# Kernel optimization log

Measured on AMD Instinct MI355X. Metric: run time of the kernel, lower is better.

Reference implementation:

```python
import jax, jax.numpy as jnp
import numpy as np

N_C, N_T, N_D = 50000, 30000, 20000
N = N_C + N_T + N_D
R = 4          # num relations
E_R = 400000   # edges per relation (contiguous blocks in edge_index)
L = 2          # num layers
H = 256        # hidden dim
EPS = 1e-5


def _layernorm(x, g, b):
    mu = jnp.mean(x, axis=-1, keepdims=True)
    var = jnp.mean(jnp.square(x - mu), axis=-1, keepdims=True)
    return (x - mu) * jax.lax.rsqrt(var + EPS) * g + b


def setup_inputs() -> dict:
    key = jax.random.key(0)
    ks = jax.random.split(key, 16)
    s = 0.02
    return {
        "x_compound": jax.random.normal(ks[0], (N_C, 256), jnp.float32),
        "x_target": jax.random.normal(ks[1], (N_T, 512), jnp.float32),
        "x_disease": jax.random.normal(ks[2], (N_D, 128), jnp.float32),
        "edge_index": jax.random.randint(ks[3], (2, R * E_R), 0, N, jnp.int32),
        "Wp_compound": jax.random.normal(ks[4], (256, H), jnp.float32) * s,
        "bp_compound": jnp.zeros((H,), jnp.float32),
        "Wp_target": jax.random.normal(ks[5], (512, H), jnp.float32) * s,
        "bp_target": jnp.zeros((H,), jnp.float32),
        "Wp_disease": jax.random.normal(ks[6], (128, H), jnp.float32) * s,
        "bp_disease": jnp.zeros((H,), jnp.float32),
        "rgcn_w": jax.random.normal(ks[7], (L, R, H, H), jnp.float32) * s,
        "rgcn_root": jax.random.normal(ks[8], (L, H, H), jnp.float32) * s,
        "rgcn_b": jnp.zeros((L, H), jnp.float32),
        "ln_g": jnp.ones((L, H), jnp.float32),
        "ln_b": jnp.zeros((L, H), jnp.float32),
        "Wo": jax.random.normal(ks[9], (H, H), jnp.float32) * s,
        "bo": jnp.zeros((H,), jnp.float32),
    }


def reference(x_compound, x_target, x_disease, edge_index,
              Wp_compound, bp_compound, Wp_target, bp_target,
              Wp_disease, bp_disease, rgcn_w, rgcn_root, rgcn_b,
              ln_g, ln_b, Wo, bo):
    # input projections per entity type, then concat (dict -> combined tensor)
    h = jnp.concatenate([
        x_compound @ Wp_compound + bp_compound,
        x_target @ Wp_target + bp_target,
        x_disease @ Wp_disease + bp_disease,
    ], axis=0)  # [N, H]

    for l in range(L):
        # RGCNConv (num_bases=None, aggr='add'): root transform + per-relation scatter-add
        out = h @ rgcn_root[l] + rgcn_b[l]
        for r in range(R):
            src = edge_index[0, r * E_R:(r + 1) * E_R]
            dst = edge_index[1, r * E_R:(r + 1) * E_R]
            msg = (h @ rgcn_w[l, r])[src]                 # [E_R, H] gather
            out = out + jax.ops.segment_sum(msg, dst, num_segments=N)
        if l > 0:  # residual only for layer_idx > 0
            out = out + h
        out = _layernorm(out, ln_g[l], ln_b[l])
        # dropout is identity in eval mode
        h = out

    y = h @ Wo + bo
    return (y[:N_C], y[N_C:N_C + N_T], y[N_C + N_T:])
```

## Files before the change

kernel.cpp:

```cpp
#include <hip/hip_runtime.h>
#include <hip/hip_bf16.h>

namespace {
constexpr int kNC = 50000;
constexpr int kNT = 30000;
constexpr int kND = 20000;
constexpr int kN  = 100000;
constexpr int kR  = 4;
constexpr int kER = 400000;
constexpr int kE  = kR * kER;
constexpr int kH  = 256;
constexpr int kB  = kR * kN;

constexpr int padM(int m) { return (m + 127) / 128 * 128; }
}

typedef __attribute__((ext_vector_type(8))) short short8;
typedef __attribute__((ext_vector_type(4))) float f32x4;
typedef __attribute__((ext_vector_type(4))) unsigned short us4;

__device__ __forceinline__ unsigned short f2bf(float x) {
    unsigned u = __builtin_bit_cast(unsigned, x);
    u += 0x7FFF + ((u >> 16) & 1);
    return (unsigned short)(u >> 16);
}
__device__ __forceinline__ float bf2f(unsigned short u) {
    unsigned v = ((unsigned)u) << 16;
    return __builtin_bit_cast(float, v);
}
__device__ __forceinline__ float bf2f_s(short u) {
    unsigned v = ((unsigned)(unsigned short)u) << 16;
    return __builtin_bit_cast(float, v);
}

__device__ __forceinline__ void gld16(const void* src, void* lds) {
    __builtin_amdgcn_global_load_lds(
        (const __attribute__((address_space(1))) void*)src,
        (__attribute__((address_space(3))) void*)lds, 16, 0, 0);
}

__device__ __forceinline__ us4 ld_u4(const unsigned short* p) {
    return *reinterpret_cast<const us4*>(p);
}
__device__ __forceinline__ void nt_store_f(float* p, float v) {
    __builtin_nontemporal_store(v, p);
}

__global__ __launch_bounds__(256)
void gemm_mfma(const unsigned short* __restrict__ A, int lda,
               const unsigned short* __restrict__ Bt, int ldb,
               const float* __restrict__ bias,
               float* __restrict__ Cf, unsigned short* __restrict__ Cb,
               int M, int K, int accumulate)
{
    __shared__ __attribute__((aligned(16))) unsigned short As[128 * 32];
    __shared__ __attribute__((aligned(16))) unsigned short Bs[128 * 32];
    const int tid  = threadIdx.x;
    const int lane = tid & 63;
    const int wid  = tid >> 6;
    const int wm   = wid >> 1;
    const int wn   = wid & 1;
    const int row0 = blockIdx.y * 128;
    const int col0 = blockIdx.x * 128;

    const int cr = lane >> 2;
    const int cs = lane & 3;

    const f32x4 z4 = {0.f, 0.f, 0.f, 0.f};
    f32x4 acc[4][4];
    #pragma unroll
    for (int m = 0; m < 4; ++m)
        #pragma unroll
        for (int n = 0; n < 4; ++n) acc[m][n] = z4;

    const int fr = lane & 15;
    const int kb = lane >> 4;

    for (int k0 = 0; k0 < K; k0 += 32) {
        #pragma unroll
        for (int j = 0; j < 2; ++j) {
            const int chunk = wid * 2 + j;
            const int r  = chunk * 16 + cr;
            const int sg = cs ^ ((r >> 1) & 3);
            gld16(A  + (size_t)(row0 + r) * lda + k0 + sg * 8, As + chunk * 512);
            gld16(Bt + (size_t)(col0 + r) * ldb + k0 + sg * 8, Bs + chunk * 512);
        }
        __syncthreads();
        short8 a[4], b[4];
        #pragma unroll
        for (int m = 0; m < 4; ++m) {
            const int am = wm * 64 + m * 16 + fr;
            const int s  = kb ^ ((am >> 1) & 3);
            a[m] = *(const short8*)(As + am * 32 + s * 8);
        }
        #pragma unroll
        for (int n = 0; n < 4; ++n) {
            const int bn = wn * 64 + n * 16 + fr;
            const int s  = kb ^ ((bn >> 1) & 3);
            b[n] = *(const short8*)(Bs + bn * 32 + s * 8);
        }
        #pragma unroll
        for (int m = 0; m < 4; ++m)
            #pragma unroll
            for (int n = 0; n < 4; ++n)
                acc[m][n] = __builtin_amdgcn_mfma_f32_16x16x32_bf16(
                    a[m], b[n], acc[m][n], 0, 0, 0);
        __syncthreads();
    }

    const int fq = lane >> 4;
    #pragma unroll
    for (int m = 0; m < 4; ++m) {
        #pragma unroll
        for (int n = 0; n < 4; ++n) {
            const int col  = col0 + wn * 64 + n * 16 + fr;
            const int rowb = row0 + wm * 64 + m * 16 + fq * 4;
            const float bv = bias ? bias[col] : 0.0f;
            #pragma unroll
            for (int i = 0; i < 4; ++i) {
                const int row = rowb + i;
                if (row >= M) continue;
                const float v = acc[m][n][i] + bv;
                const size_t idx = (size_t)row * kH + col;
                if (Cb) Cb[idx] = f2bf(v);
                else if (accumulate) Cf[idx] += v;
                else nt_store_f(&Cf[idx], v);
            }
        }
    }
}

__global__ __launch_bounds__(256, 4)
void rgcn_fused(const unsigned short* __restrict__ h_cur,
                const int* __restrict__ off, const int* __restrict__ esort,
                const unsigned short* __restrict__ W2,
                const float* __restrict__ bias, const float* __restrict__ g,
                const float* __restrict__ b,
                unsigned short* __restrict__ h_nxt, int useResid)
{
    __shared__ __attribute__((aligned(16))) unsigned short A_seg[32 * 256];
    __shared__ float red[2][4][32];
    __shared__ float gcol[256], bcol[256], biascol[256];

    const int tid  = threadIdx.x;
    const int lane = tid & 63;
    const int wid  = tid >> 6;
    const int row0 = blockIdx.x * 32;
    const int fr   = lane & 15;
    const int kb   = lane >> 4;
    const int eg   = lane >> 4;
    const int sl   = lane & 15;

    gcol[tid] = g[tid]; bcol[tid] = b[tid]; biascol[tid] = bias[tid];

    const f32x4 z4 = {0.f, 0.f, 0.f, 0.f};
    f32x4 acc[2][4];
    #pragma unroll
    for (int m = 0; m < 2; ++m)
        #pragma unroll
        for (int n = 0; n < 4; ++n) acc[m][n] = z4;

    char* const aBase = reinterpret_cast<char*>(A_seg);

    for (int p = 0; p < 5; ++p) {
        __syncthreads();
        if (p < 4) {
            int offv = 0;
            if (lane < 9) {
                int d = row0 + wid * 8 + lane;
                offv = off[(size_t)p * kN + d];
            }
            #pragma unroll
            for (int batch = 0; batch < 2; ++batch) {
                const int wrow = wid * 8 + batch * 4 + eg;
                const int t0 = __shfl(offv, batch * 4 + eg);
                const int t1 = __shfl(offv, batch * 4 + eg + 1);
                float a[16];
                #pragma unroll
                for (int i = 0; i < 16; ++i) a[i] = 0.f;
                int t = t0;
                for (; t + 2 <= t1; t += 2) {
                    const int s0 = esort[t];
                    const int s1 = esort[t + 1];
                    const short8 v0a = *reinterpret_cast<const short8*>(
                        h_cur + (size_t)s0 * kH + sl * 16);
                    const short8 v0b = *reinterpret_cast<const short8*>(
                        h_cur + (size_t)s0 * kH + sl * 16 + 8);
                    const short8 v1a = *reinterpret_cast<const short8*>(
                        h_cur + (size_t)s1 * kH + sl * 16);
                    const short8 v1b = *reinterpret_cast<const short8*>(
                        h_cur + (size_t)s1 * kH + sl * 16 + 8);
                    #pragma unroll
                    for (int i = 0; i < 8; ++i) {
                        a[i]     += bf2f_s(v0a[i]) + bf2f_s(v1a[i]);
                        a[8 + i] += bf2f_s(v0b[i]) + bf2f_s(v1b[i]);
                    }
                }
                if (t < t1) {
                    const int s0 = esort[t];
                    const short8 v0a = *reinterpret_cast<const short8*>(
                        h_cur + (size_t)s0 * kH + sl * 16);
                    const short8 v0b = *reinterpret_cast<const short8*>(
                        h_cur + (size_t)s0 * kH + sl * 16 + 8);
                    #pragma unroll
                    for (int i = 0; i < 8; ++i) {
                        a[i]     += bf2f_s(v0a[i]);
                        a[8 + i] += bf2f_s(v0b[i]);
                    }
                }
                short8 w0, w1;
                #pragma unroll
                for (int i = 0; i < 8; ++i) {
                    w0[i] = (short)f2bf(a[i]);
                    w1[i] = (short)f2bf(a[8 + i]);
                }
                const int byte0 = (wrow * 512 + sl * 32) ^ ((wrow & 7) << 4);
                *reinterpret_cast<short8*>(aBase + byte0) = w0;
                *reinterpret_cast<short8*>(aBase + (byte0 ^ 16)) = w1;
            }
        } else {
            #pragma unroll
            for (int i = 0; i < 4; ++i) {
                const int base = i * 4096 + wid * 1024;
                const int o = base + lane * 16;
                const int row = o >> 9;
                const int offr = (o & 511) ^ ((row & 7) << 4);
                gld16(h_cur + (size_t)(row0 + row) * kH + (offr >> 1), aBase + base);
            }
        }
        __syncthreads();

        const unsigned short* Wp = W2 + (size_t)p * 8 * 8192;
        #pragma unroll
        for (int ks = 0; ks < 8; ++ks) {
            const unsigned short* Wks = Wp + ks * 8192;
            const int kByte = ks * 64 + kb * 16;
            short8 a[2], bf[4];
            #pragma unroll
            for (int m = 0; m < 2; ++m) {
                const int am = m * 16 + fr;
                const int byte = (am * 512 + kByte) ^ ((am & 7) << 4);
                a[m] = *reinterpret_cast<const short8*>(aBase + byte);
            }
            #pragma unroll
            for (int n = 0; n < 4; ++n) {
                const int cn = wid * 64 + n * 16 + fr;
                bf[n] = *reinterpret_cast<const short8*>(Wks + cn * 32 + kb * 8);
            }
            #pragma unroll
            for (int m = 0; m < 2; ++m)
                #pragma unroll
                for (int n = 0; n < 4; ++n)
                    acc[m][n] = __builtin_amdgcn_mfma_f32_16x16x32_bf16(
                        a[m], bf[n], acc[m][n], 0, 0, 0);
        }
    }

    const int fq = lane >> 4;
    #pragma unroll
    for (int m = 0; m < 2; ++m) {
        #pragma unroll
        for (int i = 0; i < 4; ++i) {
            const int rowloc = m * 16 + fq * 4 + i;
            const int row = row0 + rowloc;
            float s = 0.f, q = 0.f;
            #pragma unroll
            for (int n = 0; n < 4; ++n) {
                const int col = wid * 64 + n * 16 + fr;
                float v = acc[m][n][i] + biascol[col];
                if (useResid) v += bf2f(h_cur[(size_t)row * kH + col]);
                acc[m][n][i] = v;
                s += v;
                q += v * v;
            }
            #pragma unroll
            for (int w = 1; w <= 8; w <<= 1) {
                s += __shfl_xor(s, w);
                q += __shfl_xor(q, w);
            }
            if (fr == 0) { red[0][wid][rowloc] = s; red[1][wid][rowloc] = q; }
        }
    }
    __syncthreads();
    #pragma unroll
    for (int m = 0; m < 2; ++m) {
        #pragma unroll
        for (int i = 0; i < 4; ++i) {
            const int rowloc = m * 16 + fq * 4 + i;
            const int row = row0 + rowloc;
            const float s  = red[0][0][rowloc] + red[0][1][rowloc]
                           + red[0][2][rowloc] + red[0][3][rowloc];
            const float qq = red[1][0][rowloc] + red[1][1][rowloc]
                           + red[1][2][rowloc] + red[1][3][rowloc];
            const float mu = s * (1.0f / kH);
            const float var = qq * (1.0f / kH) - mu * mu;
            const float rstd = rsqrtf(var + 1e-5f);
            #pragma unroll
            for (int n = 0; n < 4; ++n) {
                const int col = wid * 64 + n * 16 + fr;
                const float o = (acc[m][n][i] - mu) * rstd * gcol[col] + bcol[col];
                h_nxt[(size_t)row * kH + col] = f2bf(o);
            }
        }
    }
}


__global__ __launch_bounds__(256)
void conv_bf16(const float* __restrict__ in, unsigned short* __restrict__ out, int n)
{
    int i = (blockIdx.x * 256 + threadIdx.x) * 4;
    if (i >= n) return;
    f32x4 v = *reinterpret_cast<const f32x4*>(in + i);
    us4 o = { f2bf(v.x), f2bf(v.y), f2bf(v.z), f2bf(v.w) };
    *reinterpret_cast<us4*>(out + i) = o;
}

__global__ __launch_bounds__(256)
void wT_bf16(const float* __restrict__ W, unsigned short* __restrict__ Wt, int K)
{
    int t = blockIdx.x * 256 + threadIdx.x;
    if (t >= 256 * K) return;
    int c = t / K, k = t % K;
    Wt[t] = f2bf(W[(size_t)k * 256 + c]);
}

__global__ __launch_bounds__(256)
void wstack2_bf16(const float* __restrict__ w, const float* __restrict__ root,
                  unsigned short* __restrict__ W2)
{
    int t = blockIdx.x * 256 + threadIdx.x;
    if (t >= 5 * 8 * 256 * 32) return;
    const int e   = t & 7;
    const int kb  = (t >> 3) & 3;
    const int col = (t >> 5) & 255;
    const int ks  = (t >> 13) & 7;
    const int p   = t >> 16;
    const int k   = p * 256 + ks * 32 + kb * 8 + e;
    const float v = (k < 1024) ? w[(size_t)k * 256 + col]
                               : root[(size_t)(k - 1024) * 256 + col];
    W2[t] = f2bf(v);
}


__global__ __launch_bounds__(256)
void count_deg(const int* __restrict__ dst, int* __restrict__ deg, int nE)
{
    int e = blockIdx.x * 256 + threadIdx.x;
    if (e >= nE) return;
    int r = e / kER;
    atomicAdd(&deg[r * kN + dst[e]], 1);
}

__global__ __launch_bounds__(256)
void chunk_reduce(const int* __restrict__ deg, int* __restrict__ chunkSum, int B)
{
    __shared__ int sm[256];
    int s = 0;
    #pragma unroll
    for (int j = 0; j < 4; ++j) {
        int idx = blockIdx.x * 1024 + j * 256 + threadIdx.x;
        if (idx < B) s += deg[idx];
    }
    sm[threadIdx.x] = s;
    __syncthreads();
    for (int o = 128; o >= 1; o >>= 1) {
        if (threadIdx.x < o) sm[threadIdx.x] += sm[threadIdx.x + o];
        __syncthreads();
    }
    if (threadIdx.x == 0) chunkSum[blockIdx.x] = sm[0];
}

__global__ __launch_bounds__(64)
void scan_chunks(const int* __restrict__ chunkSum, int* __restrict__ chunkBase, int n)
{
    int lane = threadIdx.x;
    int base = 0;
    for (int i0 = 0; i0 < n; i0 += 64) {
        int i = i0 + lane;
        int orig = (i < n) ? chunkSum[i] : 0;
        int v = orig;
        #pragma unroll
        for (int o = 1; o < 64; o <<= 1) {
            int t = __shfl_up(v, o);
            if (lane >= o) v += t;
        }
        if (i < n) chunkBase[i] = base + v - orig;
        base += __shfl(v, 63);
    }
}

__global__ __launch_bounds__(256)
void scan_within(const int* __restrict__ deg, const int* __restrict__ chunkBase,
                 int* __restrict__ off, int B)
{
    __shared__ int ts[256];
    const int i0 = blockIdx.x * 1024;
    int v[4];
    int s = 0;
    #pragma unroll
    for (int j = 0; j < 4; ++j) {
        int idx = i0 + threadIdx.x * 4 + j;
        v[j] = (idx < B) ? deg[idx] : 0;
        s += v[j];
    }
    ts[threadIdx.x] = s;
    __syncthreads();
    for (int o = 1; o < 256; o <<= 1) {
        int u = (threadIdx.x >= o) ? ts[threadIdx.x - o] : 0;
        __syncthreads();
        ts[threadIdx.x] += u;
        __syncthreads();
    }
    int run = chunkBase[blockIdx.x] + ts[threadIdx.x] - s;
    #pragma unroll
    for (int j = 0; j < 4; ++j) {
        int idx = i0 + threadIdx.x * 4 + j;
        if (idx <= B) off[idx] = run;
        run += v[j];
    }
}

__global__ __launch_bounds__(256)
void fill_csr(const int* __restrict__ src, const int* __restrict__ dst,
              int* __restrict__ cursor, int* __restrict__ esort, int nE)
{
    int e = blockIdx.x * 256 + threadIdx.x;
    if (e >= nE) return;
    int r = e / kER;
    int pos = atomicAdd(&cursor[r * kN + dst[e]], 1);
    esort[pos] = src[e];
}


extern "C" void kernel_launch(void* const* d_in, const int* in_sizes, int n_in,
                              void* d_out, int out_size, void* d_ws, size_t ws_size,
                              hipStream_t stream)
{
    const float* x_c  = (const float*)d_in[0];
    const float* x_t  = (const float*)d_in[1];
    const float* x_d  = (const float*)d_in[2];
    const int*   ei   = (const int*)d_in[3];
    const float* Wp_c = (const float*)d_in[4];
    const float* bp_c = (const float*)d_in[5];
    const float* Wp_t = (const float*)d_in[6];
    const float* bp_t = (const float*)d_in[7];
    const float* Wp_d = (const float*)d_in[8];
    const float* bp_d = (const float*)d_in[9];
    const float* rgcn_w    = (const float*)d_in[10];
    const float* rgcn_root = (const float*)d_in[11];
    const float* rgcn_b    = (const float*)d_in[12];
    const float* ln_g = (const float*)d_in[13];
    const float* ln_b = (const float*)d_in[14];
    const float* Wo   = (const float*)d_in[15];
    const float* bo   = (const float*)d_in[16];

    const int* src_base = ei;
    const int* dst_base = ei + (size_t)kE;

    const int nChunks = (kB + 1023) / 1024;
    const int pN  = padM(kN);
    const int pNC = padM(kNC);
    const int pNT = padM(kNT);
    const int pND = padM(kND);

    char* p = (char*)d_ws;
    unsigned short* hA = (unsigned short*)p;  p += (size_t)pN * kH * 2;
    unsigned short* hB = (unsigned short*)p;  p += (size_t)pN * kH * 2;
    unsigned short* xbf_c = (unsigned short*)p;  p += (size_t)pNC * 256 * 2;
    unsigned short* xbf_t = (unsigned short*)p;  p += (size_t)pNT * 512 * 2;
    unsigned short* xbf_d = (unsigned short*)p;  p += (size_t)pND * 128 * 2;
    unsigned short* Wt_c = (unsigned short*)p;
    unsigned short* Wt_t = Wt_c + 256 * 256;
    unsigned short* Wt_d = Wt_t + 256 * 512;
    unsigned short* W2   = Wt_d + 256 * 128;
    unsigned short* Wt_o = W2 + 2 * 5 * 8 * 256 * 32;
    p = (char*)(Wt_o + 256 * 256);

    int* deg    = (int*)p;
    int* off    = deg + kB;
    int* esort  = off + (kB + 1);
    int* chunkS = esort + kE;
    int* chunkB = chunkS + 1024;

    float* outf = (float*)d_out;

    const dim3 blk(256);

    hipMemsetAsync(deg, 0, (size_t)kB * sizeof(int), stream);
    count_deg<<<dim3((kE + 255) / 256), blk, 0, stream>>>(dst_base, deg, kE);
    chunk_reduce<<<dim3(nChunks), blk, 0, stream>>>(deg, chunkS, kB);
    scan_chunks<<<dim3(1), dim3(64), 0, stream>>>(chunkS, chunkB, nChunks);
    scan_within<<<dim3(nChunks), blk, 0, stream>>>(deg, chunkB, off, kB);
    hipMemcpyAsync(deg, off, (size_t)kB * sizeof(int), hipMemcpyDeviceToDevice, stream);
    fill_csr<<<dim3((kE + 255) / 256), blk, 0, stream>>>(src_base, dst_base, deg, esort, kE);

    conv_bf16<<<dim3((kNC * 256 / 4 + 255) / 256), blk, 0, stream>>>(x_c, xbf_c, kNC * 256);
    conv_bf16<<<dim3((kNT * 512 / 4 + 255) / 256), blk, 0, stream>>>(x_t, xbf_t, kNT * 512);
    conv_bf16<<<dim3((kND * 128 / 4 + 255) / 256), blk, 0, stream>>>(x_d, xbf_d, kND * 128);
    wT_bf16<<<dim3((256 * 256 + 255) / 256), blk, 0, stream>>>(Wp_c, Wt_c, 256);
    wT_bf16<<<dim3((256 * 512 + 255) / 256), blk, 0, stream>>>(Wp_t, Wt_t, 512);
    wT_bf16<<<dim3((256 * 128 + 255) / 256), blk, 0, stream>>>(Wp_d, Wt_d, 128);
    wT_bf16<<<dim3((256 * 256 + 255) / 256), blk, 0, stream>>>(Wo, Wt_o, 256);
    for (int l = 0; l < 2; ++l)
        wstack2_bf16<<<dim3(5 * 8 * 256 * 32 / 256), blk, 0, stream>>>(
            rgcn_w + (size_t)l * kR * kH * kH, rgcn_root + (size_t)l * kH * kH,
            W2 + (size_t)l * 5 * 8 * 256 * 32);

    gemm_mfma<<<dim3(2, pNC / 128), blk, 0, stream>>>(
        xbf_c, 256, Wt_c, 256, bp_c, nullptr, hA, kNC, 256, 0);
    gemm_mfma<<<dim3(2, pNT / 128), blk, 0, stream>>>(
        xbf_t, 512, Wt_t, 512, bp_t, nullptr, hA + (size_t)kNC * kH, kNT, 512, 0);
    gemm_mfma<<<dim3(2, pND / 128), blk, 0, stream>>>(
        xbf_d, 128, Wt_d, 128, bp_d, nullptr, hA + (size_t)(kNC + kNT) * kH, kND, 128, 0);

    const dim3 fusedGrid(kN / 32);
    rgcn_fused<<<fusedGrid, blk, 0, stream>>>(
        hA, off, esort, W2, rgcn_b, ln_g, ln_b, hB, 0);
    rgcn_fused<<<fusedGrid, blk, 0, stream>>>(
        hB, off, esort, W2 + (size_t)5 * 8 * 256 * 32,
        rgcn_b + kH, ln_g + kH, ln_b + kH, hA, 1);

    gemm_mfma<<<dim3(2, pN / 128), blk, 0, stream>>>(
        hA, 256, Wt_o, 256, bo, outf, nullptr, kN, 256, 0);
}
```

Measured before the change: 848.3 us.

## Double-buffer gathered segment tiles and unroll edge gather by four

The fused RGCN kernel now uses two LDS A-tile buffers, so it gathers and sums the next relation's neighbor rows while the MFMA loop runs on the current one. One barrier per phase replaces two. The offset loads for all four relations are hoisted to kernel entry, and the edge accumulation loop is unrolled to four edges per step for more memory-level parallelism. In exchange the kernel uses twice the LDS and more registers, which may reduce occupancy under the 256x4 launch bounds.

Measured after the change: 889.1 us. 4.8% more time.

```diff
diff --git a/kernel.cpp b/kernel.cpp
--- a/kernel.cpp
+++ b/kernel.cpp
@@ -130,6 +130,54 @@
     }
 }
 
+__device__ __forceinline__ void gather_row(
+    const unsigned short* __restrict__ h_cur, const int* __restrict__ esort,
+    int t0, int t1, int wrow, int sl, char* aBase)
+{
+    float a[16];
+    #pragma unroll
+    for (int i = 0; i < 16; ++i) a[i] = 0.f;
+    int t = t0;
+    for (; t + 4 <= t1; t += 4) {
+        const int s0 = esort[t];
+        const int s1 = esort[t + 1];
+        const int s2 = esort[t + 2];
+        const int s3 = esort[t + 3];
+        const short8 v0a = *reinterpret_cast<const short8*>(h_cur + (size_t)s0 * kH + sl * 16);
+        const short8 v0b = *reinterpret_cast<const short8*>(h_cur + (size_t)s0 * kH + sl * 16 + 8);
+        const short8 v1a = *reinterpret_cast<const short8*>(h_cur + (size_t)s1 * kH + sl * 16);
+        const short8 v1b = *reinterpret_cast<const short8*>(h_cur + (size_t)s1 * kH + sl * 16 + 8);
+        const short8 v2a = *reinterpret_cast<const short8*>(h_cur + (size_t)s2 * kH + sl * 16);
+        const short8 v2b = *reinterpret_cast<const short8*>(h_cur + (size_t)s2 * kH + sl * 16 + 8);
+        const short8 v3a = *reinterpret_cast<const short8*>(h_cur + (size_t)s3 * kH + sl * 16);
+        const short8 v3b = *reinterpret_cast<const short8*>(h_cur + (size_t)s3 * kH + sl * 16 + 8);
+        #pragma unroll
+        for (int i = 0; i < 8; ++i) {
+            a[i]     += (bf2f_s(v0a[i]) + bf2f_s(v1a[i])) + (bf2f_s(v2a[i]) + bf2f_s(v3a[i]));
+            a[8 + i] += (bf2f_s(v0b[i]) + bf2f_s(v1b[i])) + (bf2f_s(v2b[i]) + bf2f_s(v3b[i]));
+        }
+    }
+    for (; t < t1; ++t) {
+        const int s0 = esort[t];
+        const short8 v0a = *reinterpret_cast<const short8*>(h_cur + (size_t)s0 * kH + sl * 16);
+        const short8 v0b = *reinterpret_cast<const short8*>(h_cur + (size_t)s0 * kH + sl * 16 + 8);
+        #pragma unroll
+        for (int i = 0; i < 8; ++i) {
+            a[i]     += bf2f_s(v0a[i]);
+            a[8 + i] += bf2f_s(v0b[i]);
+        }
+    }
+    short8 w0, w1;
+    #pragma unroll
+    for (int i = 0; i < 8; ++i) {
+        w0[i] = (short)f2bf(a[i]);
+        w1[i] = (short)f2bf(a[8 + i]);
+    }
+    const int byte0 = (wrow * 512 + sl * 32) ^ ((wrow & 7) << 4);
+    *reinterpret_cast<short8*>(aBase + byte0) = w0;
+    *reinterpret_cast<short8*>(aBase + (byte0 ^ 16)) = w1;
+}
+
 __global__ __launch_bounds__(256, 4)
 void rgcn_fused(const unsigned short* __restrict__ h_cur,
                 const int* __restrict__ off, const int* __restrict__ esort,
@@ -138,7 +186,7 @@
                 const float* __restrict__ b,
                 unsigned short* __restrict__ h_nxt, int useResid)
 {
-    __shared__ __attribute__((aligned(16))) unsigned short A_seg[32 * 256];
+    __shared__ __attribute__((aligned(16))) unsigned short A_seg[2][32 * 256];
     __shared__ float red[2][4][32];
     __shared__ float gcol[256], bcol[256], biascol[256];
 
@@ -153,6 +201,13 @@
 
     gcol[tid] = g[tid]; bcol[tid] = b[tid]; biascol[tid] = bias[tid];
 
+    int offv[4];
+    #pragma unroll
+    for (int p = 0; p < 4; ++p) {
+        offv[p] = 0;
+        if (lane < 9) offv[p] = off[(size_t)p * kN + row0 + wid * 8 + lane];
+    }
+
     const f32x4 z4 = {0.f, 0.f, 0.f, 0.f};
     f32x4 acc[2][4];
     #pragma unroll
@@ -160,63 +215,14 @@
         #pragma unroll
         for (int n = 0; n < 4; ++n) acc[m][n] = z4;
 
-    char* const aBase = reinterpret_cast<char*>(A_seg);
-
-    for (int p = 0; p < 5; ++p) {
-        __syncthreads();
-        if (p < 4) {
-            int offv = 0;
-            if (lane < 9) {
-                int d = row0 + wid * 8 + lane;
-                offv = off[(size_t)p * kN + d];
-            }
+    auto fill = [&](int q, char* aBase) {
+        if (q < 4) {
             #pragma unroll
             for (int batch = 0; batch < 2; ++batch) {
                 const int wrow = wid * 8 + batch * 4 + eg;
-                const int t0 = __shfl(offv, batch * 4 + eg);
-                const int t1 = __shfl(offv, batch * 4 + eg + 1);
-                float a[16];
-                #pragma unroll
-                for (int i = 0; i < 16; ++i) a[i] = 0.f;
-                int t = t0;
-                for (; t + 2 <= t1; t += 2) {
-                    const int s0 = esort[t];
-                    const int s1 = esort[t + 1];
-                    const short8 v0a = *reinterpret_cast<const short8*>(
-                        h_cur + (size_t)s0 * kH + sl * 16);
-                    const short8 v0b = *reinterpret_cast<const short8*>(
-                        h_cur + (size_t)s0 * kH + sl * 16 + 8);
-                    const short8 v1a = *reinterpret_cast<const short8*>(
-                        h_cur + (size_t)s1 * kH + sl * 16);
-                    const short8 v1b = *reinterpret_cast<const short8*>(
-                        h_cur + (size_t)s1 * kH + sl * 16 + 8);
-                    #pragma unroll
-                    for (int i = 0; i < 8; ++i) {
-                        a[i]     += bf2f_s(v0a[i]) + bf2f_s(v1a[i]);
-                        a[8 + i] += bf2f_s(v0b[i]) + bf2f_s(v1b[i]);
-                    }
-                }
-                if (t < t1) {
-                    const int s0 = esort[t];
-                    const short8 v0a = *reinterpret_cast<const short8*>(
-                        h_cur + (size_t)s0 * kH + sl * 16);
-                    const short8 v0b = *reinterpret_cast<const short8*>(
-                        h_cur + (size_t)s0 * kH + sl * 16 + 8);
-                    #pragma unroll
-                    for (int i = 0; i < 8; ++i) {
-                        a[i]     += bf2f_s(v0a[i]);
-                        a[8 + i] += bf2f_s(v0b[i]);
-                    }
-                }
-                short8 w0, w1;
-                #pragma unroll
-                for (int i = 0; i < 8; ++i) {
-                    w0[i] = (short)f2bf(a[i]);
-                    w1[i] = (short)f2bf(a[8 + i]);
-                }
-                const int byte0 = (wrow * 512 + sl * 32) ^ ((wrow & 7) << 4);
-                *reinterpret_cast<short8*>(aBase + byte0) = w0;
-                *reinterpret_cast<short8*>(aBase + (byte0 ^ 16)) = w1;
+                const int t0 = __shfl(offv[q], batch * 4 + eg);
+                const int t1 = __shfl(offv[q], batch * 4 + eg + 1);
+                gather_row(h_cur, esort, t0, t1, wrow, sl, aBase);
             }
         } else {
             #pragma unroll
@@ -228,8 +234,15 @@
                 gld16(h_cur + (size_t)(row0 + row) * kH + (offr >> 1), aBase + base);
             }
         }
-        __syncthreads();
-
+    };
+
+    fill(0, reinterpret_cast<char*>(A_seg[0]));
+    __syncthreads();
+
+    for (int p = 0; p < 5; ++p) {
+        if (p < 4) fill(p + 1, reinterpret_cast<char*>(A_seg[(p + 1) & 1]));
+
+        char* const aBase = reinterpret_cast<char*>(A_seg[p & 1]);
         const unsigned short* Wp = W2 + (size_t)p * 8 * 8192;
         #pragma unroll
         for (int ks = 0; ks < 8; ++ks) {
@@ -254,6 +267,7 @@
                     acc[m][n] = __builtin_amdgcn_mfma_f32_16x16x32_bf16(
                         a[m], bf[n], acc[m][n], 0, 0, 0);
         }
+        __syncthreads();
     }
 
     const int fq = lane >> 4;
```
